# Performance work log

Measured on AMD Instinct MI355X. Metric: run time of the kernel, lower is better.

The kernel has to match this reference:

```python
import jax, jax.numpy as jnp
import numpy as np

FC = 2048      # fc_feat_size
VEMB = 512     # video_embedding_size
WEMB = 512     # word_embedding_size
H = 512        # lstm_hidden_size
A = 256        # att_hidden_size
TV = 32        # video_time_step
TC = 20        # caption_time_step
BC = 16        # batch_size_caption
RP = 32        # rp_num (proposals per caption)
B = BC * RP    # batch_size
GLOVE = 300


def setup_inputs() -> dict:
    key = jax.random.key(0)
    ks = jax.random.split(key, 12)
    def u(k, shape):
        return jax.random.uniform(k, shape, jnp.float32, -0.1, 0.1)
    def n(k, shape, s=0.05):
        return jax.random.normal(k, shape, jnp.float32) * s
    return {
        "video_fc_feat": jax.random.normal(ks[0], (B, TV, FC), jnp.float32),
        "video_caption": jax.random.normal(ks[1], (BC, TC, GLOVE), jnp.float32),
        "cap_length_list": jax.random.randint(ks[2], (BC,), 0, TC),
        # video_embedding / word_embedding (Linear layers)
        "W_vemb": u(ks[3], (VEMB, FC)), "b_vemb": jnp.zeros((VEMB,), jnp.float32),
        "W_wemb": u(ks[4], (WEMB, GLOVE)), "b_wemb": jnp.zeros((WEMB,), jnp.float32),
        # LSTMCell for video (gate order i,f,g,o as in torch)
        "Wih_v": n(ks[5], (4 * H, VEMB)), "Whh_v": n(ks[6], (4 * H, H)),
        "bih_v": jnp.zeros((4 * H,), jnp.float32), "bhh_v": jnp.zeros((4 * H,), jnp.float32),
        # LSTMCell for caption
        "Wih_c": n(ks[7], (4 * H, WEMB)), "Whh_c": n(ks[8], (4 * H, H)),
        "bih_c": jnp.zeros((4 * H,), jnp.float32), "bhh_c": jnp.zeros((4 * H,), jnp.float32),
        # attention linears
        "W_vid": u(ks[9], (A, H)), "b_vid": jnp.zeros((A,), jnp.float32),
        "W_sen": u(ks[10], (A, H)), "b_sen": jnp.zeros((A,), jnp.float32),
        "W_att": u(ks[11], (1, A)), "b_att": jnp.zeros((1,), jnp.float32),
    }


def _lstm(x_seq, Wih, Whh, bih, bhh):
    # x_seq: [B, T, D] -> hidden states [B, T, H]; torch LSTMCell gate order i,f,g,o
    Bb = x_seq.shape[0]
    Hh = Whh.shape[1]
    def step(carry, x):
        h, c = carry
        g = x @ Wih.T + bih + h @ Whh.T + bhh
        i, f, gg, o = jnp.split(g, 4, axis=-1)
        c = jax.nn.sigmoid(f) * c + jax.nn.sigmoid(i) * jnp.tanh(gg)
        h = jax.nn.sigmoid(o) * jnp.tanh(c)
        return (h, c), h
    init = (jnp.zeros((Bb, Hh), x_seq.dtype), jnp.zeros((Bb, Hh), x_seq.dtype))
    _, hs = jax.lax.scan(step, init, jnp.swapaxes(x_seq, 0, 1))
    return jnp.swapaxes(hs, 0, 1)


def reference(video_fc_feat, video_caption, cap_length_list,
              W_vemb, b_vemb, W_wemb, b_wemb,
              Wih_v, Whh_v, bih_v, bhh_v,
              Wih_c, Whh_c, bih_c, bhh_c,
              W_vid, b_vid, W_sen, b_sen, W_att, b_att):
    Bb, TVv, _ = video_fc_feat.shape
    BCc, TCc, _ = video_caption.shape
    rp = Bb // BCc
    Hh = Whh_v.shape[1]

    # caption LSTM over embedded GloVe words
    cap_x = video_caption @ W_wemb.T + b_wemb                 # [BC, TC, WEMB]
    cap_h = _lstm(cap_x, Wih_c, Whh_c, bih_c, bhh_c)          # [BC, TC, H]
    # video LSTM over embedded fc features
    vid_x = video_fc_feat @ W_vemb.T + b_vemb                 # [B, TV, VEMB]
    vid_h = _lstm(vid_x, Wih_v, Whh_v, bih_v, bhh_v)          # [B, TV, H]

    # additive attention: tanh(vid_linear(h_v) + sen_linear(h_c)) -> att_linear
    c_lin = cap_h @ W_sen.T + b_sen                           # [BC, TC, A]
    v_lin = (vid_h @ W_vid.T + b_vid).reshape(BCc, rp, TVv, -1)  # [BC, RP, TV, A]
    scores = (jnp.tanh(v_lin[:, :, :, None, :] + c_lin[:, None, None, :, :])
              @ W_att.T + b_att)[..., 0]                      # [BC, RP, TV, TC]

    # ragged masked softmax over caption length (max(len, 1) as in original)
    cap_len = jnp.maximum(cap_length_list, 1)
    mask = jnp.arange(TCc)[None, :] < cap_len[:, None]        # [BC, TC]
    m = mask[:, None, None, :]
    w = jax.nn.softmax(jnp.where(m, scores, -1e9), axis=-1)
    w = jnp.where(m, w, 0.0)                                  # [BC, RP, TV, TC]

    att_cap = jnp.einsum('brvt,bth->brvh', w, cap_h)          # [BC, RP, TV, H]
    cap_ftr_mean = att_cap.mean(axis=2)                       # mean over video steps
    vid_mean = vid_h.mean(axis=1).reshape(BCc, rp, Hh)
    return (vid_mean, cap_ftr_mean)
```

## Files before the change

### kernel.cpp

```cpp
#include <hip/hip_runtime.h>
#include <hip/hip_bf16.h>

#define FCD 2048
#define VEMBD 512
#define WEMBD 512
#define HD 512
#define AD 256
#define TVD 32
#define TCD 20
#define BCD 16
#define RPD 32
#define BD 512
#define GLOVED 300

typedef __attribute__((ext_vector_type(8))) short short8v;
typedef __attribute__((ext_vector_type(4))) float f32x4;

__device__ __forceinline__ float sigf(float x) { return 1.0f / (1.0f + __expf(-x)); }
__device__ __forceinline__ float tanhfast(float x) {
    float e = __expf(2.0f * x);
    return 1.0f - 2.0f / (e + 1.0f);
}
__device__ __forceinline__ unsigned short f2bf(float x) {
    union { __hip_bfloat16 h; unsigned short u; } v;
    v.h = __float2bfloat16(x);
    return v.u;
}
__device__ __forceinline__ float b2f(unsigned short u) {
    union { unsigned int i; float f; } v;
    v.i = ((unsigned int)u) << 16;
    return v.f;
}

__launch_bounds__(256)
__global__ void conv_f2b_kernel(const float* __restrict__ src,
                                unsigned short* __restrict__ dst, int n4) {
    for (int i = blockIdx.x * 256 + threadIdx.x; i < n4; i += gridDim.x * 256) {
        const float4 v = ((const float4*)src)[i];
        ushort4 o;
        o.x = f2bf(v.x); o.y = f2bf(v.y); o.z = f2bf(v.z); o.w = f2bf(v.w);
        ((ushort4*)dst)[i] = o;
    }
}

__launch_bounds__(256)
__global__ void conv_wcat_perm_kernel(const float* __restrict__ Wih,
                                      const float* __restrict__ Whh,
                                      unsigned short* __restrict__ Wcat) {
    const int gp = blockIdx.x;
    const int q = (gp >> 4) & 3;
    const int hc = (gp >> 6) * 16 + (gp & 15);
    const long g = (long)(q * 512 + hc);
    for (int k = threadIdx.x; k < 512; k += 256) {
        Wcat[(long)gp * 1024 + k]       = f2bf(Wih[g * 512 + k]);
        Wcat[(long)gp * 1024 + 512 + k] = f2bf(Whh[g * 512 + k]);
    }
}

__launch_bounds__(256)
__global__ void conv_bsum_kernel(const float* __restrict__ bih,
                                 const float* __restrict__ bhh,
                                 float* __restrict__ bsum) {
    const int gp = blockIdx.x * 256 + threadIdx.x;
    if (gp < 2048) {
        const int q = (gp >> 4) & 3;
        const int hc = (gp >> 6) * 16 + (gp & 15);
        const int g = q * 512 + hc;
        bsum[gp] = bih[g] + bhh[g];
    }
}

template<int AF32, int OBF>
__launch_bounds__(256)
__global__ void mfma_gemm128(const void* __restrict__ A,
                             const unsigned short* __restrict__ Bw,
                             const float* __restrict__ bias,
                             void* __restrict__ Cout,
                             int M, int N, int K)
{
    __shared__ unsigned short As[128][40];
    __shared__ unsigned short Bs[128][40];
    const int m0 = blockIdx.x * 128;
    const int n0 = blockIdx.y * 128;
    const int tid = threadIdx.x;
    const int lane = tid & 63;
    const int wid = tid >> 6;
    const int wm = (wid >> 1) * 64;
    const int wn = (wid & 1) * 64;
    const int lrow = lane & 15;
    const int lko = (lane >> 4) * 8;

    f32x4 acc[4][4] = {};

    for (int k0 = 0; k0 < K; k0 += 32) {
#pragma unroll
        for (int i = 0; i < 2; i++) {
            const int chunk = tid + i * 256;
            const int r = chunk >> 2;
            const int c8 = (chunk & 3) * 8;
            if (AF32) {
                const float* Af = (const float*)A + (long)(m0 + r) * K + k0 + c8;
                const float4 v0 = *(const float4*)Af;
                const float4 v1 = *(const float4*)(Af + 4);
                unsigned short* d = &As[r][c8];
                d[0] = f2bf(v0.x); d[1] = f2bf(v0.y); d[2] = f2bf(v0.z); d[3] = f2bf(v0.w);
                d[4] = f2bf(v1.x); d[5] = f2bf(v1.y); d[6] = f2bf(v1.z); d[7] = f2bf(v1.w);
            } else {
                *(short8v*)&As[r][c8] =
                    *(const short8v*)((const unsigned short*)A + (long)(m0 + r) * K + k0 + c8);
            }
            *(short8v*)&Bs[r][c8] =
                *(const short8v*)(Bw + (long)(n0 + r) * K + k0 + c8);
        }
        __syncthreads();
        short8v a[4], b[4];
#pragma unroll
        for (int mi = 0; mi < 4; mi++)
            a[mi] = *(const short8v*)&As[wm + mi * 16 + lrow][lko];
#pragma unroll
        for (int ni = 0; ni < 4; ni++)
            b[ni] = *(const short8v*)&Bs[wn + ni * 16 + lrow][lko];
#pragma unroll
        for (int mi = 0; mi < 4; mi++)
#pragma unroll
            for (int ni = 0; ni < 4; ni++)
                acc[mi][ni] = __builtin_amdgcn_mfma_f32_16x16x32_bf16(
                    a[mi], b[ni], acc[mi][ni], 0, 0, 0);
        __syncthreads();
    }

    const int rbase = (lane >> 4) * 4;
#pragma unroll
    for (int ni = 0; ni < 4; ni++) {
        const int col = n0 + wn + ni * 16 + lrow;
        const float bv = bias[col];
#pragma unroll
        for (int mi = 0; mi < 4; mi++) {
#pragma unroll
            for (int j = 0; j < 4; j++) {
                const long row = m0 + wm + mi * 16 + rbase + j;
                const float val = acc[mi][ni][j] + bv;
                if (OBF) ((unsigned short*)Cout)[row * N + col] = f2bf(val);
                else     ((float*)Cout)[row * N + col] = val;
            }
        }
    }
}

__launch_bounds__(256)
__global__ void vid_step_mfma(const unsigned short* __restrict__ vx,
                              const unsigned short* __restrict__ h_in,
                              const unsigned short* __restrict__ Wcat,
                              const float* __restrict__ bsum,
                              float* __restrict__ c_state,
                              unsigned short* __restrict__ h_out,
                              unsigned short* __restrict__ vid_h,
                              int t)
{
    __shared__ unsigned short As[64][136];
    __shared__ unsigned short Ws2[64][136];
    const int n0 = blockIdx.x * 64;
    const int b0 = blockIdx.y * 64;
    const int tid = threadIdx.x;
    const int lane = tid & 63;
    const int w = tid >> 6;
    const int lrow = lane & 15;
    const int lko = (lane >> 4) * 8;
    const int sr = tid >> 2;
    const int sc = (tid & 3) * 32;

    f32x4 acc[4] = {};

    const unsigned short* arow_vx = vx + ((long)(b0 + sr) * TVD + t) * 512;
    const unsigned short* arow_h  = h_in + (long)(b0 + sr) * 512;
    const unsigned short* wrow    = Wcat + (long)(n0 + sr) * 1024;

#pragma unroll
    for (int i = 0; i < 4; i++) {
        *(short8v*)&As[sr][sc + i * 8]  = *(const short8v*)(arow_vx + sc + i * 8);
        *(short8v*)&Ws2[sr][sc + i * 8] = *(const short8v*)(wrow + sc + i * 8);
    }
    __syncthreads();

    short8v pa[4], pw[4];
    for (int c = 0; c < 8; c++) {
        if (c < 7) {
            const int k0 = (c + 1) * 128;
            const unsigned short* ap = (k0 < 512) ? (arow_vx + k0 + sc)
                                                  : (arow_h + (k0 - 512) + sc);
            const unsigned short* wp = wrow + k0 + sc;
#pragma unroll
            for (int i = 0; i < 4; i++) {
                pa[i] = *(const short8v*)(ap + i * 8);
                pw[i] = *(const short8v*)(wp + i * 8);
            }
        }
#pragma unroll
        for (int kk = 0; kk < 4; kk++) {
            const short8v a = *(const short8v*)&As[w * 16 + lrow][kk * 32 + lko];
#pragma unroll
            for (int ni = 0; ni < 4; ni++) {
                const short8v b = *(const short8v*)&Ws2[ni * 16 + lrow][kk * 32 + lko];
                acc[ni] = __builtin_amdgcn_mfma_f32_16x16x32_bf16(a, b, acc[ni], 0, 0, 0);
            }
        }
        __syncthreads();
        if (c < 7) {
#pragma unroll
            for (int i = 0; i < 4; i++) {
                *(short8v*)&As[sr][sc + i * 8]  = pa[i];
                *(short8v*)&Ws2[sr][sc + i * 8] = pw[i];
            }
            __syncthreads();
        }
    }

    const int hc = (n0 >> 2) + lrow;
    const int rbase = (lane >> 4) * 4;
    const float bs0 = bsum[n0 + lrow];
    const float bs1 = bsum[n0 + 16 + lrow];
    const float bs2 = bsum[n0 + 32 + lrow];
    const float bs3 = bsum[n0 + 48 + lrow];
#pragma unroll
    for (int j = 0; j < 4; j++) {
        const long b = b0 + w * 16 + rbase + j;
        const float gi = acc[0][j] + bs0;
        const float gf = acc[1][j] + bs1;
        const float gg = acc[2][j] + bs2;
        const float go = acc[3][j] + bs3;
        const float c_old = c_state[b * 512 + hc];
        const float ii = sigf(gi), ff = sigf(gf), g2 = tanhfast(gg), oo = sigf(go);
        const float cn = ff * c_old + ii * g2;
        const float h = oo * tanhfast(cn);
        c_state[b * 512 + hc] = cn;
        h_out[b * 512 + hc] = f2bf(h);
        vid_h[(b * TVD + t) * 512 + hc] = f2bf(h);
    }
}

__launch_bounds__(256)
__global__ void gemm_bias_kernel(const float* __restrict__ A,
                                 const float* __restrict__ Bw,
                                 const float* __restrict__ bias,
                                 float* __restrict__ C,
                                 int M, int N, int K) {
    __shared__ float As[16][68];
    __shared__ float Bs[16][68];
    const int n0 = blockIdx.x * 64;
    const int m0 = blockIdx.y * 64;
    const int tid = threadIdx.x;
    const int tx = tid & 15;
    const int ty = tid >> 4;
    const int lrow = tid >> 2;
    const int lk4 = (tid & 3) * 4;

    float acc[4][4] = {};

    for (int k0 = 0; k0 < K; k0 += 16) {
        {
            const float* src = A + (long)(m0 + lrow) * K + k0 + lk4;
            float4 v;
            if (k0 + 16 <= K) v = *(const float4*)src;
            else {
                v.x = (k0 + lk4 + 0 < K) ? src[0] : 0.f;
                v.y = (k0 + lk4 + 1 < K) ? src[1] : 0.f;
                v.z = (k0 + lk4 + 2 < K) ? src[2] : 0.f;
                v.w = (k0 + lk4 + 3 < K) ? src[3] : 0.f;
            }
            As[lk4 + 0][lrow] = v.x; As[lk4 + 1][lrow] = v.y;
            As[lk4 + 2][lrow] = v.z; As[lk4 + 3][lrow] = v.w;
        }
        {
            const float* src = Bw + (long)(n0 + lrow) * K + k0 + lk4;
            float4 v;
            if (k0 + 16 <= K) v = *(const float4*)src;
            else {
                v.x = (k0 + lk4 + 0 < K) ? src[0] : 0.f;
                v.y = (k0 + lk4 + 1 < K) ? src[1] : 0.f;
                v.z = (k0 + lk4 + 2 < K) ? src[2] : 0.f;
                v.w = (k0 + lk4 + 3 < K) ? src[3] : 0.f;
            }
            Bs[lk4 + 0][lrow] = v.x; Bs[lk4 + 1][lrow] = v.y;
            Bs[lk4 + 2][lrow] = v.z; Bs[lk4 + 3][lrow] = v.w;
        }
        __syncthreads();
#pragma unroll
        for (int kk = 0; kk < 16; kk++) {
            const float4 av = *(const float4*)&As[kk][ty * 4];
            const float4 bv = *(const float4*)&Bs[kk][tx * 4];
            acc[0][0] += av.x * bv.x; acc[0][1] += av.x * bv.y; acc[0][2] += av.x * bv.z; acc[0][3] += av.x * bv.w;
            acc[1][0] += av.y * bv.x; acc[1][1] += av.y * bv.y; acc[1][2] += av.y * bv.z; acc[1][3] += av.y * bv.w;
            acc[2][0] += av.z * bv.x; acc[2][1] += av.z * bv.y; acc[2][2] += av.z * bv.z; acc[2][3] += av.z * bv.w;
            acc[3][0] += av.w * bv.x; acc[3][1] += av.w * bv.y; acc[3][2] += av.w * bv.z; acc[3][3] += av.w * bv.w;
        }
        __syncthreads();
    }

    const float b0v = bias[n0 + tx * 4 + 0];
    const float b1v = bias[n0 + tx * 4 + 1];
    const float b2v = bias[n0 + tx * 4 + 2];
    const float b3v = bias[n0 + tx * 4 + 3];
#pragma unroll
    for (int i = 0; i < 4; i++) {
        float* dst = C + (long)(m0 + ty * 4 + i) * N + n0 + tx * 4;
        dst[0] = acc[i][0] + b0v;
        dst[1] = acc[i][1] + b1v;
        dst[2] = acc[i][2] + b2v;
        dst[3] = acc[i][3] + b3v;
    }
}

__launch_bounds__(256)
__global__ void cap_step_kernel(const float* __restrict__ xg,
                                const float* __restrict__ Whh,
                                const float* __restrict__ bhh,
                                const float* __restrict__ h_in,
                                float* __restrict__ h_out,
                                float* __restrict__ c_state,
                                float* __restrict__ cap_h,
                                int t)
{
    __shared__ float Ws[64][68];
    __shared__ float Hsh[16][68];
    const int h0 = blockIdx.x * 16;
    const int tid = threadIdx.x;
    const int tx = tid & 15;
    const int ty = tid >> 4;
    const int lrow = tid >> 2;
    const int lq = tid & 3;

    float acc[4] = {};

    for (int k0 = 0; k0 < 512; k0 += 64) {
        {
            const int q = lrow >> 4;
            const int hcc = lrow & 15;
            const float* src = Whh + (long)(q * 512 + h0 + hcc) * 512 + k0 + lq * 16;
            const int col = hcc * 4 + q;
#pragma unroll
            for (int j = 0; j < 4; j++) {
                const float4 v = *(const float4*)(src + j * 4);
                Ws[lq * 16 + j * 4 + 0][col] = v.x;
                Ws[lq * 16 + j * 4 + 1][col] = v.y;
                Ws[lq * 16 + j * 4 + 2][col] = v.z;
                Ws[lq * 16 + j * 4 + 3][col] = v.w;
            }
        }
        {
            const int lb = tid >> 4;
            const int lk4 = (tid & 15) * 4;
            *(float4*)&Hsh[lb][lk4] = *(const float4*)(h_in + (long)lb * 512 + k0 + lk4);
        }
        __syncthreads();
#pragma unroll
        for (int kq = 0; kq < 16; kq++) {
            const float4 h4 = *(const float4*)&Hsh[ty][kq * 4];
            const float4 w0 = *(const float4*)&Ws[kq * 4 + 0][tx * 4];
            const float4 w1 = *(const float4*)&Ws[kq * 4 + 1][tx * 4];
            const float4 w2 = *(const float4*)&Ws[kq * 4 + 2][tx * 4];
            const float4 w3 = *(const float4*)&Ws[kq * 4 + 3][tx * 4];
            acc[0] += h4.x * w0.x + h4.y * w1.x + h4.z * w2.x + h4.w * w3.x;
            acc[1] += h4.x * w0.y + h4.y * w1.y + h4.z * w2.y + h4.w * w3.y;
            acc[2] += h4.x * w0.z + h4.y * w1.z + h4.z * w2.z + h4.w * w3.z;
            acc[3] += h4.x * w0.w + h4.y * w1.w + h4.z * w2.w + h4.w * w3.w;
        }
        __syncthreads();
    }

    const int hc = h0 + tx;
    const long xrow = (long)(ty * TCD + t) * 2048;
    const float gi = acc[0] + xg[xrow + hc]        + bhh[hc];
    const float gf = acc[1] + xg[xrow + 512 + hc]  + bhh[512 + hc];
    const float gg = acc[2] + xg[xrow + 1024 + hc] + bhh[1024 + hc];
    const float go = acc[3] + xg[xrow + 1536 + hc] + bhh[1536 + hc];
    const float c_old = c_state[(long)ty * 512 + hc];
    const float ii = sigf(gi), ff = sigf(gf), g2 = tanhfast(gg), oo = sigf(go);
    const float c = ff * c_old + ii * g2;
    const float h = oo * tanhfast(c);
    c_state[(long)ty * 512 + hc] = c;
    h_out[(long)ty * 512 + hc] = h;
    cap_h[(long)(ty * TCD + t) * 512 + hc] = h;
}

__launch_bounds__(256)
__global__ void attn_kernel(const float* __restrict__ v_lin,
                            const float* __restrict__ c_lin,
                            const float* __restrict__ W_att,
                            const float* __restrict__ b_att,
                            const int* __restrict__ cap_len,
                            float* __restrict__ wbar)
{
    const int br = blockIdx.x;
    const int bc = br >> 5;
    const int tid = threadIdx.x;
    const int lane = tid & 63;
    const int wv = tid >> 6;
    __shared__ float cl[TCD][AD];
    __shared__ float vl[AD];
    __shared__ float sl[TVD][TCD];

    for (int tt = 0; tt < TCD; tt++)
        cl[tt][tid] = c_lin[(long)(bc * TCD + tt) * AD + tid];
    const float wa0 = W_att[lane];
    const float wa1 = W_att[64 + lane];
    const float wa2 = W_att[128 + lane];
    const float wa3 = W_att[192 + lane];
    const float batt = b_att[0];
    __syncthreads();

    for (int v = 0; v < TVD; v++) {
        vl[tid] = v_lin[((long)br * TVD + v) * AD + tid];
        __syncthreads();
        const float v0 = vl[lane], v1 = vl[64 + lane], v2 = vl[128 + lane], v3 = vl[192 + lane];
#pragma unroll
        for (int dt = 0; dt < 5; dt++) {
            const int t = wv * 5 + dt;
            float s = tanhfast(v0 + cl[t][lane]) * wa0
                    + tanhfast(v1 + cl[t][64 + lane]) * wa1
                    + tanhfast(v2 + cl[t][128 + lane]) * wa2
                    + tanhfast(v3 + cl[t][192 + lane]) * wa3;
            for (int off = 32; off > 0; off >>= 1) s += __shfl_down(s, off, 64);
            if (lane == 0) sl[v][t] = s + batt;
        }
        __syncthreads();
    }

    int L = cap_len[bc];
    if (L < 1) L = 1;
    if (tid < TVD) {
        const int v = tid;
        float m = -1e30f;
        for (int t = 0; t < TCD; t++)
            if (t < L) m = fmaxf(m, sl[v][t]);
        float sum = 0.f;
        for (int t = 0; t < TCD; t++)
            if (t < L) sum += __expf(sl[v][t] - m);
        const float inv = 1.f / sum;
        for (int t = 0; t < TCD; t++)
            sl[v][t] = (t < L) ? __expf(sl[v][t] - m) * inv : 0.f;
    }
    __syncthreads();
    if (tid < TCD) {
        float s = 0.f;
        for (int v = 0; v < TVD; v++) s += sl[v][tid];
        wbar[(long)br * TCD + tid] = s * (1.0f / TVD);
    }
}

__launch_bounds__(256)
__global__ void capftr_kernel(const float* __restrict__ wbar,
                              const float* __restrict__ cap_h,
                              float* __restrict__ out2)
{
    const int idx = blockIdx.x * 256 + threadIdx.x;
    const int h = idx & 511;
    const int br = idx >> 9;
    const int bc = br >> 5;
    float s = 0.f;
#pragma unroll
    for (int t = 0; t < TCD; t++)
        s += wbar[br * TCD + t] * cap_h[(long)(bc * TCD + t) * HD + h];
    out2[idx] = s;
}

__launch_bounds__(256)
__global__ void vidmean_bf_kernel(const unsigned short* __restrict__ vid_h,
                                  float* __restrict__ out1)
{
    const int idx = blockIdx.x * 256 + threadIdx.x;
    const int b = idx >> 6;
    const int h8 = (idx & 63) * 8;
    float s[8] = {};
    for (int t = 0; t < TVD; t++) {
        const short8v v = *(const short8v*)(vid_h + ((long)b * TVD + t) * 512 + h8);
#pragma unroll
        for (int j = 0; j < 8; j++) s[j] += b2f((unsigned short)v[j]);
    }
#pragma unroll
    for (int j = 0; j < 8; j++)
        out1[(long)b * 512 + h8 + j] = s[j] * (1.0f / TVD);
}

extern "C" void kernel_launch(void* const* d_in, const int* in_sizes, int n_in,
                              void* d_out, int out_size, void* d_ws, size_t ws_size,
                              hipStream_t stream) {
    const float* video_fc      = (const float*)d_in[0];
    const float* video_caption = (const float*)d_in[1];
    const int*   cap_len       = (const int*)d_in[2];
    const float* W_vemb = (const float*)d_in[3];
    const float* b_vemb = (const float*)d_in[4];
    const float* W_wemb = (const float*)d_in[5];
    const float* b_wemb = (const float*)d_in[6];
    const float* Wih_v  = (const float*)d_in[7];
    const float* Whh_v  = (const float*)d_in[8];
    const float* bih_v  = (const float*)d_in[9];
    const float* bhh_v  = (const float*)d_in[10];
    const float* Wih_c  = (const float*)d_in[11];
    const float* Whh_c  = (const float*)d_in[12];
    const float* bih_c  = (const float*)d_in[13];
    const float* bhh_c  = (const float*)d_in[14];
    const float* W_vid  = (const float*)d_in[15];
    const float* b_vid  = (const float*)d_in[16];
    const float* W_sen  = (const float*)d_in[17];
    const float* b_sen  = (const float*)d_in[18];
    const float* W_att  = (const float*)d_in[19];
    const float* b_att  = (const float*)d_in[20];

    float* out1 = (float*)d_out;
    float* out2 = out1 + BD * HD;

    float* ws = (float*)d_ws;
    size_t off = 0;
    auto alloc = [&](size_t nfloats) {
        float* p = ws + off;
        off += (nfloats + 63) & ~(size_t)63;
        return p;
    };
    unsigned short* vidx_bf = (unsigned short*)alloc((size_t)BD * TVD * VEMBD / 2);
    unsigned short* vidh_bf = (unsigned short*)alloc((size_t)BD * TVD * HD / 2);
    unsigned short* h_bf_a  = (unsigned short*)alloc((size_t)BD * HD / 2);
    unsigned short* h_bf_b  = (unsigned short*)alloc((size_t)BD * HD / 2);
    float* c_st    = alloc((size_t)BD * HD);
    float* v_lin   = alloc((size_t)BD * TVD * AD);
    unsigned short* Wvemb_bf = (unsigned short*)alloc((size_t)VEMBD * FCD / 2);
    unsigned short* Wvid_bf  = (unsigned short*)alloc((size_t)AD * HD / 2);
    unsigned short* Wcat_bf  = (unsigned short*)alloc((size_t)2048 * 1024 / 2);
    float* bsum    = alloc(2048);
    float* cap_x   = alloc((size_t)BCD * TCD * WEMBD);
    float* xg_c    = alloc((size_t)BCD * TCD * 4 * HD);
    float* cap_h   = alloc((size_t)BCD * TCD * HD);
    float* c_lin   = alloc((size_t)BCD * TCD * AD);
    float* wbar    = alloc((size_t)BD * TCD);
    float* cap_ha  = alloc((size_t)BCD * HD);
    float* cap_hb  = alloc((size_t)BCD * HD);
    float* cap_cst = alloc((size_t)BCD * HD);

    hipMemsetAsync(h_bf_a, 0, (size_t)BD * HD * sizeof(unsigned short), stream);
    hipMemsetAsync(c_st, 0, (size_t)BD * HD * sizeof(float), stream);
    hipMemsetAsync(cap_ha, 0, (size_t)BCD * HD * sizeof(float), stream);
    hipMemsetAsync(cap_cst, 0, (size_t)BCD * HD * sizeof(float), stream);

    conv_f2b_kernel<<<512, 256, 0, stream>>>(W_vemb, Wvemb_bf, VEMBD * FCD / 4);
    conv_f2b_kernel<<<128, 256, 0, stream>>>(W_vid, Wvid_bf, AD * HD / 4);
    conv_wcat_perm_kernel<<<2048, 256, 0, stream>>>(Wih_v, Whh_v, Wcat_bf);
    conv_bsum_kernel<<<8, 256, 0, stream>>>(bih_v, bhh_v, bsum);

    gemm_bias_kernel<<<dim3(WEMBD / 64, (BCD * TCD) / 64), 256, 0, stream>>>(
        video_caption, W_wemb, b_wemb, cap_x, BCD * TCD, WEMBD, GLOVED);
    gemm_bias_kernel<<<dim3((4 * HD) / 64, (BCD * TCD) / 64), 256, 0, stream>>>(
        cap_x, Wih_c, bih_c, xg_c, BCD * TCD, 4 * HD, WEMBD);
    for (int t = 0; t < TCD; t++) {
        const float* hin = (t & 1) ? cap_hb : cap_ha;
        float* hout = (t & 1) ? cap_ha : cap_hb;
        cap_step_kernel<<<32, 256, 0, stream>>>(xg_c, Whh_c, bhh_c, hin, hout, cap_cst, cap_h, t);
    }
    gemm_bias_kernel<<<dim3(AD / 64, (BCD * TCD) / 64), 256, 0, stream>>>(
        cap_h, W_sen, b_sen, c_lin, BCD * TCD, AD, HD);

    mfma_gemm128<1, 1><<<dim3((BD * TVD) / 128, VEMBD / 128), 256, 0, stream>>>(
        video_fc, Wvemb_bf, b_vemb, vidx_bf, BD * TVD, VEMBD, FCD);
    for (int t = 0; t < TVD; t++) {
        const unsigned short* hin = (t & 1) ? h_bf_b : h_bf_a;
        unsigned short* hout = (t & 1) ? h_bf_a : h_bf_b;
        vid_step_mfma<<<dim3(2048 / 64, BD / 64), 256, 0, stream>>>(
            vidx_bf, hin, Wcat_bf, bsum, c_st, hout, vidh_bf, t);
    }
    mfma_gemm128<0, 0><<<dim3((BD * TVD) / 128, AD / 128), 256, 0, stream>>>(
        vidh_bf, Wvid_bf, b_vid, v_lin, BD * TVD, AD, HD);

    attn_kernel<<<BD, 256, 0, stream>>>(v_lin, c_lin, W_att, b_att, cap_len, wbar);
    capftr_kernel<<<(BD * HD) / 256, 256, 0, stream>>>(wbar, cap_h, out2);
    vidmean_bf_kernel<<<(BD * HD / 8) / 256, 256, 0, stream>>>(vidh_bf, out1);
}
```

Baseline: 1.003 ms.

## Fuse caption and video LSTM steps into one launch, split-K video step

Caption LSTM steps now run as extra blocks inside the per-timestep video LSTM kernel, which removes the 20 separate caption launches and lets the two recurrences share the GPU. The video step uses 512 threads split into two K-halves (input path and hidden path) that reduce through shared memory, halving the serial K loop per block. The 128x128 MFMA GEMM now uses 64-wide K tiles with register prefetch double-buffering. The cost is more shared memory per block (68KB), which can lower occupancy, and an extra reduction sync in the video step.

```diff
diff --git a/kernel.cpp b/kernel.cpp
--- a/kernel.cpp
+++ b/kernel.cpp
@@ -78,8 +78,8 @@
                              void* __restrict__ Cout,
                              int M, int N, int K)
 {
-    __shared__ unsigned short As[128][40];
-    __shared__ unsigned short Bs[128][40];
+    __shared__ unsigned short As[128][72];
+    __shared__ unsigned short Bs[128][72];
     const int m0 = blockIdx.x * 128;
     const int n0 = blockIdx.y * 128;
     const int tid = threadIdx.x;
@@ -89,44 +89,86 @@
     const int wn = (wid & 1) * 64;
     const int lrow = lane & 15;
     const int lko = (lane >> 4) * 8;
+    const int sr = tid >> 1;
+    const int sc = (tid & 1) * 32;
 
     f32x4 acc[4][4] = {};
 
-    for (int k0 = 0; k0 < K; k0 += 32) {
-#pragma unroll
-        for (int i = 0; i < 2; i++) {
-            const int chunk = tid + i * 256;
-            const int r = chunk >> 2;
-            const int c8 = (chunk & 3) * 8;
+    const float* Arow_f = (const float*)A + (long)(m0 + sr) * K;
+    const unsigned short* Arow_b = (const unsigned short*)A + (long)(m0 + sr) * K;
+    const unsigned short* Brow = Bw + (long)(n0 + sr) * K;
+
+    if (AF32) {
+#pragma unroll
+        for (int i = 0; i < 8; i++) {
+            const float4 v = *(const float4*)(Arow_f + sc + i * 4);
+            unsigned short* d = &As[sr][sc + i * 4];
+            d[0] = f2bf(v.x); d[1] = f2bf(v.y); d[2] = f2bf(v.z); d[3] = f2bf(v.w);
+        }
+    } else {
+#pragma unroll
+        for (int i = 0; i < 4; i++)
+            *(short8v*)&As[sr][sc + i * 8] = *(const short8v*)(Arow_b + sc + i * 8);
+    }
+#pragma unroll
+    for (int i = 0; i < 4; i++)
+        *(short8v*)&Bs[sr][sc + i * 8] = *(const short8v*)(Brow + sc + i * 8);
+    __syncthreads();
+
+    const int nc = K >> 6;
+    float4 paf[8];
+    short8v pab[4], pb[4];
+    for (int c = 0; c < nc; c++) {
+        if (c < nc - 1) {
+            const int k0 = (c + 1) * 64;
             if (AF32) {
-                const float* Af = (const float*)A + (long)(m0 + r) * K + k0 + c8;
-                const float4 v0 = *(const float4*)Af;
-                const float4 v1 = *(const float4*)(Af + 4);
-                unsigned short* d = &As[r][c8];
-                d[0] = f2bf(v0.x); d[1] = f2bf(v0.y); d[2] = f2bf(v0.z); d[3] = f2bf(v0.w);
-                d[4] = f2bf(v1.x); d[5] = f2bf(v1.y); d[6] = f2bf(v1.z); d[7] = f2bf(v1.w);
+#pragma unroll
+                for (int i = 0; i < 8; i++)
+                    paf[i] = *(const float4*)(Arow_f + k0 + sc + i * 4);
             } else {
-                *(short8v*)&As[r][c8] =
-                    *(const short8v*)((const unsigned short*)A + (long)(m0 + r) * K + k0 + c8);
-            }
-            *(short8v*)&Bs[r][c8] =
-                *(const short8v*)(Bw + (long)(n0 + r) * K + k0 + c8);
+#pragma unroll
+                for (int i = 0; i < 4; i++)
+                    pab[i] = *(const short8v*)(Arow_b + k0 + sc + i * 8);
+            }
+#pragma unroll
+            for (int i = 0; i < 4; i++)
+                pb[i] = *(const short8v*)(Brow + k0 + sc + i * 8);
+        }
+#pragma unroll
+        for (int kk = 0; kk < 2; kk++) {
+            short8v a[4], b[4];
+#pragma unroll
+            for (int mi = 0; mi < 4; mi++)
+                a[mi] = *(const short8v*)&As[wm + mi * 16 + lrow][kk * 32 + lko];
+#pragma unroll
+            for (int ni = 0; ni < 4; ni++)
+                b[ni] = *(const short8v*)&Bs[wn + ni * 16 + lrow][kk * 32 + lko];
+#pragma unroll
+            for (int mi = 0; mi < 4; mi++)
+#pragma unroll
+                for (int ni = 0; ni < 4; ni++)
+                    acc[mi][ni] = __builtin_amdgcn_mfma_f32_16x16x32_bf16(
+                        a[mi], b[ni], acc[mi][ni], 0, 0, 0);
         }
         __syncthreads();
-        short8v a[4], b[4];
-#pragma unroll
-        for (int mi = 0; mi < 4; mi++)
-            a[mi] = *(const short8v*)&As[wm + mi * 16 + lrow][lko];
-#pragma unroll
-        for (int ni = 0; ni < 4; ni++)
-            b[ni] = *(const short8v*)&Bs[wn + ni * 16 + lrow][lko];
-#pragma unroll
-        for (int mi = 0; mi < 4; mi++)
-#pragma unroll
-            for (int ni = 0; ni < 4; ni++)
-                acc[mi][ni] = __builtin_amdgcn_mfma_f32_16x16x32_bf16(
-                    a[mi], b[ni], acc[mi][ni], 0, 0, 0);
-        __syncthreads();
+        if (c < nc - 1) {
+            if (AF32) {
+#pragma unroll
+                for (int i = 0; i < 8; i++) {
+                    unsigned short* d = &As[sr][sc + i * 4];
+                    d[0] = f2bf(paf[i].x); d[1] = f2bf(paf[i].y);
+                    d[2] = f2bf(paf[i].z); d[3] = f2bf(paf[i].w);
+                }
+            } else {
+#pragma unroll
+                for (int i = 0; i < 4; i++)
+                    *(short8v*)&As[sr][sc + i * 8] = pab[i];
+            }
+#pragma unroll
+            for (int i = 0; i < 4; i++)
+                *(short8v*)&Bs[sr][sc + i * 8] = pb[i];
+            __syncthreads();
+        }
     }
 
     const int rbase = (lane >> 4) * 4;
@@ -147,94 +189,190 @@
     }
 }
 
-__launch_bounds__(256)
-__global__ void vid_step_mfma(const unsigned short* __restrict__ vx,
-                              const unsigned short* __restrict__ h_in,
-                              const unsigned short* __restrict__ Wcat,
-                              const float* __restrict__ bsum,
-                              float* __restrict__ c_state,
-                              unsigned short* __restrict__ h_out,
-                              unsigned short* __restrict__ vid_h,
-                              int t)
+__launch_bounds__(512)
+__global__ void step_fused(const unsigned short* __restrict__ vx,
+                           const unsigned short* __restrict__ h_in,
+                           unsigned short* __restrict__ h_out,
+                           const unsigned short* __restrict__ Wcat,
+                           const float* __restrict__ bsum,
+                           float* __restrict__ c_state,
+                           unsigned short* __restrict__ vid_h,
+                           int t,
+                           const float* __restrict__ xg,
+                           const float* __restrict__ Whh_c,
+                           const float* __restrict__ bhh_c,
+                           const float* __restrict__ hc_in,
+                           float* __restrict__ hc_out,
+                           float* __restrict__ cap_cst,
+                           float* __restrict__ cap_h)
 {
-    __shared__ unsigned short As[64][136];
-    __shared__ unsigned short Ws2[64][136];
-    const int n0 = blockIdx.x * 64;
-    const int b0 = blockIdx.y * 64;
+    __shared__ __align__(16) unsigned char smem[69632];
+    const int bx = blockIdx.x;
     const int tid = threadIdx.x;
+
+    if (bx >= 256) {
+        const int h0 = (bx - 256) * 16;
+        float* Wsc = (float*)smem;
+        float* Hshc = (float*)(smem + 17408);
+        const int lrow = tid >> 3;
+        const int lq8 = tid & 7;
+        const int tx = tid & 15;
+        const int ty = (tid >> 4) & 15;
+        float acc4[4] = {};
+
+        for (int k0 = 0; k0 < 512; k0 += 64) {
+            {
+                const int q = lrow >> 4;
+                const int hcc = lrow & 15;
+                const float* src = Whh_c + (long)(q * 512 + h0 + hcc) * 512 + k0 + lq8 * 8;
+                const int col = hcc * 4 + q;
+#pragma unroll
+                for (int j = 0; j < 2; j++) {
+                    const float4 v = *(const float4*)(src + j * 4);
+                    Wsc[(lq8 * 8 + j * 4 + 0) * 68 + col] = v.x;
+                    Wsc[(lq8 * 8 + j * 4 + 1) * 68 + col] = v.y;
+                    Wsc[(lq8 * 8 + j * 4 + 2) * 68 + col] = v.z;
+                    Wsc[(lq8 * 8 + j * 4 + 3) * 68 + col] = v.w;
+                }
+            }
+            if (tid < 256) {
+                const int lb = tid >> 4;
+                const int lk4 = (tid & 15) * 4;
+                *(float4*)&Hshc[lb * 68 + lk4] = *(const float4*)(hc_in + (long)lb * 512 + k0 + lk4);
+            }
+            __syncthreads();
+            if (tid < 256) {
+#pragma unroll
+                for (int kq = 0; kq < 16; kq++) {
+                    const float4 h4 = *(const float4*)&Hshc[ty * 68 + kq * 4];
+                    const float4 w0 = *(const float4*)&Wsc[(kq * 4 + 0) * 68 + tx * 4];
+                    const float4 w1 = *(const float4*)&Wsc[(kq * 4 + 1) * 68 + tx * 4];
+                    const float4 w2 = *(const float4*)&Wsc[(kq * 4 + 2) * 68 + tx * 4];
+                    const float4 w3 = *(const float4*)&Wsc[(kq * 4 + 3) * 68 + tx * 4];
+                    acc4[0] += h4.x * w0.x + h4.y * w1.x + h4.z * w2.x + h4.w * w3.x;
+                    acc4[1] += h4.x * w0.y + h4.y * w1.y + h4.z * w2.y + h4.w * w3.y;
+                    acc4[2] += h4.x * w0.z + h4.y * w1.z + h4.z * w2.z + h4.w * w3.z;
+                    acc4[3] += h4.x * w0.w + h4.y * w1.w + h4.z * w2.w + h4.w * w3.w;
+                }
+            }
+            __syncthreads();
+        }
+        if (tid < 256) {
+            const int hc = h0 + tx;
+            const long xrow = (long)(ty * TCD + t) * 2048;
+            const float gi = acc4[0] + xg[xrow + hc]        + bhh_c[hc];
+            const float gf = acc4[1] + xg[xrow + 512 + hc]  + bhh_c[512 + hc];
+            const float gg = acc4[2] + xg[xrow + 1024 + hc] + bhh_c[1024 + hc];
+            const float go = acc4[3] + xg[xrow + 1536 + hc] + bhh_c[1536 + hc];
+            const float c_old = cap_cst[(long)ty * 512 + hc];
+            const float ii = sigf(gi), ff = sigf(gf), g2 = tanhfast(gg), oo = sigf(go);
+            const float c = ff * c_old + ii * g2;
+            const float h = oo * tanhfast(c);
+            cap_cst[(long)ty * 512 + hc] = c;
+            hc_out[(long)ty * 512 + hc] = h;
+            cap_h[(long)(ty * TCD + t) * 512 + hc] = h;
+        }
+        return;
+    }
+
+    const int n0 = (bx & 31) * 64;
+    const int b0 = (bx >> 5) * 64;
     const int lane = tid & 63;
-    const int w = tid >> 6;
+    const int wl = (tid >> 6) & 3;
+    const int g = tid >> 8;
     const int lrow = lane & 15;
     const int lko = (lane >> 4) * 8;
-    const int sr = tid >> 2;
-    const int sc = (tid & 3) * 32;
-
-    f32x4 acc[4] = {};
+    const int sr = tid >> 3;
+    const int sc = (tid & 7) * 16;
+
+    unsigned short* As0 = (unsigned short*)smem;
+    unsigned short* Ws0 = (unsigned short*)(smem + 17408);
+    unsigned short* As1 = (unsigned short*)(smem + 34816);
+    unsigned short* Ws1 = (unsigned short*)(smem + 52224);
+    unsigned short* Asg = (unsigned short*)(smem + g * 34816);
+    unsigned short* Wsg = Asg + 17408 / 2;
 
     const unsigned short* arow_vx = vx + ((long)(b0 + sr) * TVD + t) * 512;
     const unsigned short* arow_h  = h_in + (long)(b0 + sr) * 512;
     const unsigned short* wrow    = Wcat + (long)(n0 + sr) * 1024;
 
-#pragma unroll
-    for (int i = 0; i < 4; i++) {
-        *(short8v*)&As[sr][sc + i * 8]  = *(const short8v*)(arow_vx + sc + i * 8);
-        *(short8v*)&Ws2[sr][sc + i * 8] = *(const short8v*)(wrow + sc + i * 8);
+    f32x4 acc[4] = {};
+
+#pragma unroll
+    for (int i = 0; i < 2; i++) {
+        *(short8v*)&As0[sr * 136 + sc + i * 8] = *(const short8v*)(arow_vx + sc + i * 8);
+        *(short8v*)&Ws0[sr * 136 + sc + i * 8] = *(const short8v*)(wrow + sc + i * 8);
+        *(short8v*)&As1[sr * 136 + sc + i * 8] = *(const short8v*)(arow_h + sc + i * 8);
+        *(short8v*)&Ws1[sr * 136 + sc + i * 8] = *(const short8v*)(wrow + 512 + sc + i * 8);
     }
     __syncthreads();
 
-    short8v pa[4], pw[4];
-    for (int c = 0; c < 8; c++) {
-        if (c < 7) {
-            const int k0 = (c + 1) * 128;
-            const unsigned short* ap = (k0 < 512) ? (arow_vx + k0 + sc)
-                                                  : (arow_h + (k0 - 512) + sc);
-            const unsigned short* wp = wrow + k0 + sc;
-#pragma unroll
-            for (int i = 0; i < 4; i++) {
-                pa[i] = *(const short8v*)(ap + i * 8);
-                pw[i] = *(const short8v*)(wp + i * 8);
+    short8v pa0[2], pw0[2], pa1[2], pw1[2];
+    for (int p = 0; p < 4; p++) {
+        if (p < 3) {
+            const int k0 = (p + 1) * 128;
+#pragma unroll
+            for (int i = 0; i < 2; i++) {
+                pa0[i] = *(const short8v*)(arow_vx + k0 + sc + i * 8);
+                pw0[i] = *(const short8v*)(wrow + k0 + sc + i * 8);
+                pa1[i] = *(const short8v*)(arow_h + k0 + sc + i * 8);
+                pw1[i] = *(const short8v*)(wrow + 512 + k0 + sc + i * 8);
             }
         }
 #pragma unroll
         for (int kk = 0; kk < 4; kk++) {
-            const short8v a = *(const short8v*)&As[w * 16 + lrow][kk * 32 + lko];
+            const short8v a = *(const short8v*)&Asg[(wl * 16 + lrow) * 136 + kk * 32 + lko];
 #pragma unroll
             for (int ni = 0; ni < 4; ni++) {
-                const short8v b = *(const short8v*)&Ws2[ni * 16 + lrow][kk * 32 + lko];
+                const short8v b = *(const short8v*)&Wsg[(ni * 16 + lrow) * 136 + kk * 32 + lko];
                 acc[ni] = __builtin_amdgcn_mfma_f32_16x16x32_bf16(a, b, acc[ni], 0, 0, 0);
             }
         }
         __syncthreads();
-        if (c < 7) {
-#pragma unroll
-            for (int i = 0; i < 4; i++) {
-                *(short8v*)&As[sr][sc + i * 8]  = pa[i];
-                *(short8v*)&Ws2[sr][sc + i * 8] = pw[i];
+        if (p < 3) {
+#pragma unroll
+            for (int i = 0; i < 2; i++) {
+                *(short8v*)&As0[sr * 136 + sc + i * 8] = pa0[i];
+                *(short8v*)&Ws0[sr * 136 + sc + i * 8] = pw0[i];
+                *(short8v*)&As1[sr * 136 + sc + i * 8] = pa1[i];
+                *(short8v*)&Ws1[sr * 136 + sc + i * 8] = pw1[i];
             }
             __syncthreads();
         }
     }
 
-    const int hc = (n0 >> 2) + lrow;
-    const int rbase = (lane >> 4) * 4;
-    const float bs0 = bsum[n0 + lrow];
-    const float bs1 = bsum[n0 + 16 + lrow];
-    const float bs2 = bsum[n0 + 32 + lrow];
-    const float bs3 = bsum[n0 + 48 + lrow];
-#pragma unroll
-    for (int j = 0; j < 4; j++) {
-        const long b = b0 + w * 16 + rbase + j;
-        const float gi = acc[0][j] + bs0;
-        const float gf = acc[1][j] + bs1;
-        const float gg = acc[2][j] + bs2;
-        const float go = acc[3][j] + bs3;
-        const float c_old = c_state[b * 512 + hc];
-        const float ii = sigf(gi), ff = sigf(gf), g2 = tanhfast(gg), oo = sigf(go);
-        const float cn = ff * c_old + ii * g2;
-        const float h = oo * tanhfast(cn);
-        c_state[b * 512 + hc] = cn;
-        h_out[b * 512 + hc] = f2bf(h);
-        vid_h[(b * TVD + t) * 512 + hc] = f2bf(h);
+    float* red = (float*)(smem + 34816);
+    const int flat = wl * 64 + lane;
+    if (g == 1) {
+#pragma unroll
+        for (int ni = 0; ni < 4; ni++)
+#pragma unroll
+            for (int j = 0; j < 4; j++)
+                red[(ni * 4 + j) * 256 + flat] = acc[ni][j];
+    }
+    __syncthreads();
+    if (g == 0) {
+        const int hc = (n0 >> 2) + lrow;
+        const int rbase = (lane >> 4) * 4;
+        const float bs0 = bsum[n0 + lrow];
+        const float bs1 = bsum[n0 + 16 + lrow];
+        const float bs2 = bsum[n0 + 32 + lrow];
+        const float bs3 = bsum[n0 + 48 + lrow];
+#pragma unroll
+        for (int j = 0; j < 4; j++) {
+            const long b = b0 + wl * 16 + rbase + j;
+            const float gi = acc[0][j] + red[(0 * 4 + j) * 256 + flat] + bs0;
+            const float gf = acc[1][j] + red[(1 * 4 + j) * 256 + flat] + bs1;
+            const float gg = acc[2][j] + red[(2 * 4 + j) * 256 + flat] + bs2;
+            const float go = acc[3][j] + red[(3 * 4 + j) * 256 + flat] + bs3;
+            const float c_old = c_state[b * 512 + hc];
+            const float ii = sigf(gi), ff = sigf(gf), g2 = tanhfast(gg), oo = sigf(go);
+            const float cn = ff * c_old + ii * g2;
+            const float h = oo * tanhfast(cn);
+            c_state[b * 512 + hc] = cn;
+            h_out[b * 512 + hc] = f2bf(h);
+            vid_h[(b * TVD + t) * 512 + hc] = f2bf(h);
+        }
     }
 }
 
@@ -308,78 +446,6 @@
         dst[2] = acc[i][2] + b2v;
         dst[3] = acc[i][3] + b3v;
     }
-}
-
-__launch_bounds__(256)
-__global__ void cap_step_kernel(const float* __restrict__ xg,
-                                const float* __restrict__ Whh,
-                                const float* __restrict__ bhh,
-                                const float* __restrict__ h_in,
-                                float* __restrict__ h_out,
-                                float* __restrict__ c_state,
-                                float* __restrict__ cap_h,
-                                int t)
-{
-    __shared__ float Ws[64][68];
-    __shared__ float Hsh[16][68];
-    const int h0 = blockIdx.x * 16;
-    const int tid = threadIdx.x;
-    const int tx = tid & 15;
-    const int ty = tid >> 4;
-    const int lrow = tid >> 2;
-    const int lq = tid & 3;
-
-    float acc[4] = {};
-
-    for (int k0 = 0; k0 < 512; k0 += 64) {
-        {
-            const int q = lrow >> 4;
-            const int hcc = lrow & 15;
-            const float* src = Whh + (long)(q * 512 + h0 + hcc) * 512 + k0 + lq * 16;
-            const int col = hcc * 4 + q;
-#pragma unroll
-            for (int j = 0; j < 4; j++) {
-                const float4 v = *(const float4*)(src + j * 4);
-                Ws[lq * 16 + j * 4 + 0][col] = v.x;
-                Ws[lq * 16 + j * 4 + 1][col] = v.y;
-                Ws[lq * 16 + j * 4 + 2][col] = v.z;
-                Ws[lq * 16 + j * 4 + 3][col] = v.w;
-            }
-        }
-        {
-            const int lb = tid >> 4;
-            const int lk4 = (tid & 15) * 4;
-            *(float4*)&Hsh[lb][lk4] = *(const float4*)(h_in + (long)lb * 512 + k0 + lk4);
-        }
-        __syncthreads();
-#pragma unroll
-        for (int kq = 0; kq < 16; kq++) {
-            const float4 h4 = *(const float4*)&Hsh[ty][kq * 4];
-            const float4 w0 = *(const float4*)&Ws[kq * 4 + 0][tx * 4];
-            const float4 w1 = *(const float4*)&Ws[kq * 4 + 1][tx * 4];
-            const float4 w2 = *(const float4*)&Ws[kq * 4 + 2][tx * 4];
-            const float4 w3 = *(const float4*)&Ws[kq * 4 + 3][tx * 4];
-            acc[0] += h4.x * w0.x + h4.y * w1.x + h4.z * w2.x + h4.w * w3.x;
-            acc[1] += h4.x * w0.y + h4.y * w1.y + h4.z * w2.y + h4.w * w3.y;
-            acc[2] += h4.x * w0.z + h4.y * w1.z + h4.z * w2.z + h4.w * w3.z;
-            acc[3] += h4.x * w0.w + h4.y * w1.w + h4.z * w2.w + h4.w * w3.w;
-        }
-        __syncthreads();
-    }
-
-    const int hc = h0 + tx;
-    const long xrow = (long)(ty * TCD + t) * 2048;
-    const float gi = acc[0] + xg[xrow + hc]        + bhh[hc];
-    const float gf = acc[1] + xg[xrow + 512 + hc]  + bhh[512 + hc];
-    const float gg = acc[2] + xg[xrow + 1024 + hc] + bhh[1024 + hc];
-    const float go = acc[3] + xg[xrow + 1536 + hc] + bhh[1536 + hc];
-    const float c_old = c_state[(long)ty * 512 + hc];
-    const float ii = sigf(gi), ff = sigf(gf), g2 = tanhfast(gg), oo = sigf(go);
-    const float c = ff * c_old + ii * g2;
-    const float h = oo * tanhfast(c);
-    c_state[(long)ty * 512 + hc] = c;
-    h_out[(long)ty * 512 + hc] = h;
-    cap_h[(long)(ty * TCD + t) * 512 + hc] = h;
 }
 
 __launch_bounds__(256)
@@ -549,22 +615,23 @@
         video_caption, W_wemb, b_wemb, cap_x, BCD * TCD, WEMBD, GLOVED);
     gemm_bias_kernel<<<dim3((4 * HD) / 64, (BCD * TCD) / 64), 256, 0, stream>>>(
         cap_x, Wih_c, bih_c, xg_c, BCD * TCD, 4 * HD, WEMBD);
-    for (int t = 0; t < TCD; t++) {
-        const float* hin = (t & 1) ? cap_hb : cap_ha;
-        float* hout = (t & 1) ? cap_ha : cap_hb;
-        cap_step_kernel<<<32, 256, 0, stream>>>(xg_c, Whh_c, bhh_c, hin, hout, cap_cst, cap_h, t);
-    }
-    gemm_bias_kernel<<<dim3(AD / 64, (BCD * TCD) / 64), 256, 0, stream>>>(
-        cap_h, W_sen, b_sen, c_lin, BCD * TCD, AD, HD);
 
     mfma_gemm128<1, 1><<<dim3((BD * TVD) / 128, VEMBD / 128), 256, 0, stream>>>(
         video_fc, Wvemb_bf, b_vemb, vidx_bf, BD * TVD, VEMBD, FCD);
+
     for (int t = 0; t < TVD; t++) {
         const unsigned short* hin = (t & 1) ? h_bf_b : h_bf_a;
         unsigned short* hout = (t & 1) ? h_bf_a : h_bf_b;
-        vid_step_mfma<<<dim3(2048 / 64, BD / 64), 256, 0, stream>>>(
-            vidx_bf, hin, Wcat_bf, bsum, c_st, hout, vidh_bf, t);
-    }
+        const float* chin = (t & 1) ? cap_hb : cap_ha;
+        float* chout = (t & 1) ? cap_ha : cap_hb;
+        const int nblk = (t < TCD) ? 288 : 256;
+        step_fused<<<nblk, 512, 0, stream>>>(
+            vidx_bf, hin, hout, Wcat_bf, bsum, c_st, vidh_bf, t,
+            xg_c, Whh_c, bhh_c, chin, chout, cap_cst, cap_h);
+    }
+
+    gemm_bias_kernel<<<dim3(AD / 64, (BCD * TCD) / 64), 256, 0, stream>>>(
+        cap_h, W_sen, b_sen, c_lin, BCD * TCD, AD, HD);
     mfma_gemm128<0, 0><<<dim3((BD * TVD) / 128, AD / 128), 256, 0, stream>>>(
         vidh_bf, Wvid_bf, b_vid, v_lin, BD * TVD, AD, HD);
 
```

After: 884.2 us. 11.9% less time.
